# Performance work log

Measured on AMD Instinct MI355X. Metric: run time of the kernel, lower is better.

The kernel has to match this reference:

```python
import jax, jax.numpy as jnp
import numpy as np

N = 8192
D = 2048      # input_dim
DH = 1024     # input_dim // r
DO = 1024     # output_dim

def setup_inputs() -> dict:
    key = jax.random.key(0)
    ks = jax.random.split(key, 11)
    s_in = 1.0 / np.sqrt(D)
    s_h = 1.0 / np.sqrt(DH)
    return {
        "O0": jax.random.normal(ks[0], (N, D), dtype=jnp.float32),
        "Ww": jax.random.uniform(ks[1], (DH, D), jnp.float32, -s_in, s_in),
        "Wb": jax.random.uniform(ks[2], (DH,), jnp.float32, -s_in, s_in),
        "Uw": jax.random.uniform(ks[3], (DH, D), jnp.float32, -s_in, s_in),
        "Ub": jax.random.uniform(ks[4], (DH,), jnp.float32, -s_in, s_in),
        "Hw": jax.random.uniform(ks[5], (DH, D), jnp.float32, -s_in, s_in),
        "Hb": jax.random.uniform(ks[6], (DH,), jnp.float32, -s_in, s_in),
        "fc0w": jax.random.uniform(ks[7], (D, DH), jnp.float32, -s_h, s_h),
        "fc0b": jax.random.uniform(ks[8], (D,), jnp.float32, -s_h, s_h),
        "fc1w": jax.random.uniform(ks[9], (DO, D), jnp.float32, -s_in, s_in),
        "fc1b": jax.random.uniform(ks[10], (DO,), jnp.float32, -s_in, s_in),
    }

def reference(O0, Ww, Wb, Uw, Ub, Hw, Hb, fc0w, fc0b, fc1w, fc1b):
    q = O0 @ Ww.T + Wb              # [N, DH]
    k = O0 @ Uw.T + Ub              # [N, DH]
    v = O0 @ Hw.T + Hb              # [N, DH]
    scores = q @ k.T                # [N, N], unscaled as in the original
    R1 = jax.nn.softmax(scores, axis=1)
    ctx = R1 @ v                    # [N, DH]
    O1 = O0 + (ctx @ fc0w.T + fc0b) # residual, [N, D]
    O2 = O1 @ fc1w.T + fc1b         # [N, DO]
    return (O1, O2)
```

## Files before the change

kernel.cpp:

```cpp
#include <hip/hip_runtime.h>
#include <cstdint>
#include <cstddef>

typedef _Float16 f16;
typedef _Float16 f16x8 __attribute__((ext_vector_type(8)));
typedef _Float16 f16x4 __attribute__((ext_vector_type(4)));
typedef float    f32x4 __attribute__((ext_vector_type(4)));

template <int V> struct IC { static constexpr int v = V; };

template <int CTRL>
__device__ __forceinline__ float dppf(float x) {
  union { float f; int i; } u, r;
  u.f = x;
  r.i = __builtin_amdgcn_update_dpp(0, u.i, CTRL, 0xF, 0xF, true);
  return r.f;
}

__global__ __launch_bounds__(256) void cvt_f32_f16(const float* __restrict__ in,
                                                   f16* __restrict__ out, int n) {
  int i = (blockIdx.x * 256 + threadIdx.x) * 4;
  if (i < n) {
    float4 v = *(const float4*)(in + i);
    f16x4 h; h[0] = (f16)v.x; h[1] = (f16)v.y; h[2] = (f16)v.z; h[3] = (f16)v.w;
    *(f16x4*)(out + i) = h;
  }
}

__global__ __launch_bounds__(256) void cvt5_f32_f16(
    const float* __restrict__ i0, const float* __restrict__ i1,
    const float* __restrict__ i2, const float* __restrict__ i3,
    const float* __restrict__ i4, f16* __restrict__ out, int nper) {
  const int bpr = nper >> 10;
  const int r = blockIdx.x / bpr;
  const int b = blockIdx.x - r * bpr;
  const float* in = r == 0 ? i0 : r == 1 ? i1 : r == 2 ? i2 : r == 3 ? i3 : i4;
  int i = (b * 256 + threadIdx.x) * 4;
  float4 v = *(const float4*)(in + i);
  f16x4 h; h[0] = (f16)v.x; h[1] = (f16)v.y; h[2] = (f16)v.z; h[3] = (f16)v.w;
  *(f16x4*)(out + (size_t)r * nper + i) = h;
}

__global__ __launch_bounds__(256) void transpose_f16(const f16* __restrict__ in,
                                                     int ldi,
                                                     f16* __restrict__ out,
                                                     int R, int C) {
  __shared__ f16 tile[64][65];
  const int r0 = blockIdx.y * 64, c0 = blockIdx.x * 64;
  const int t = threadIdx.x;
#pragma unroll
  for (int p = 0; p < 2; p++) {
    int s = t + p * 256;
    int r = s >> 3, q = s & 7;
    const int kl = ((r & 3) << 4) + (r >> 2);
    f16x8 v = *(const f16x8*)(in + (size_t)(r0 + kl) * ldi + c0 + q * 8);
#pragma unroll
    for (int e = 0; e < 8; e++) tile[r][q * 8 + e] = v[e];
  }
  __syncthreads();
#pragma unroll
  for (int p = 0; p < 2; p++) {
    int s = t + p * 256;
    int r = s >> 3, q = s & 7;
    f16x8 v;
#pragma unroll
    for (int e = 0; e < 8; e++) v[e] = tile[q * 8 + e][r];
    *(f16x8*)(out + (size_t)(c0 + r) * R + r0 + q * 8) = v;
  }
}

template <int MODE>
__global__ __launch_bounds__(512, 2) void gemm256(
    const f16* __restrict__ A, const f16* __restrict__ B,
    int M, int N, int K, int lda, int ldb,
    const float* __restrict__ bias,
    f16* __restrict__ outH, int ldo,
    float* __restrict__ statsM, float* __restrict__ statsS, int sld,
    const float* __restrict__ alphaT,
    const float* __restrict__ resid, int ldr,
    float* __restrict__ outF, int ldof) {
  __shared__ f16 lA[2][2][128 * 64];
  __shared__ f16 lB[2][2][128 * 64];
  __shared__ float lAl[2][256];

  const int t = threadIdx.x;
  const int wave = t >> 6, lane = t & 63;
  const int wr = wave >> 2, wc = wave & 3;
  const int quad = lane >> 4, l16 = lane & 15;
  const int rc = lane >> 3;
  const int kcs = (lane & 7) ^ rc;

  const int nwg = gridDim.x * gridDim.y;
  const int bid = blockIdx.y * gridDim.x + blockIdx.x;
  const int sb = (bid & 7) * (nwg >> 3) + (bid >> 3);
  const int bx = sb % gridDim.x, by = sb / gridDim.x;
  const int m0 = by * 256, n0 = bx * 256;
  const int nk = K >> 6;

  const f16* Abase = A + (size_t)m0 * lda;
  const f16* Bbase = B + (size_t)n0 * ldb;

  auto stageA = [&](int tau, int h) {
    if (tau >= nk) return;
    const f16* src = Abase + (size_t)(h * 128 + rc) * lda + tau * 64 + kcs * 8;
    f16* dstu = &lA[tau & 1][h][0];
#pragma unroll
    for (int j = 0; j < 2; j++) {
      const int sl = j * 8 + wave;
      __builtin_amdgcn_global_load_lds(
          (const __attribute__((address_space(1))) void*)(src + (size_t)sl * 8 * lda),
          (__attribute__((address_space(3))) void*)(dstu + sl * 512), 16, 0, 0);
    }
  };
  auto stageB = [&](int tau, int h) {
    if (tau >= nk) return;
    const f16* src = Bbase + (size_t)(h * 128 + rc) * ldb + tau * 64 + kcs * 8;
    f16* dstu = &lB[tau & 1][h][0];
#pragma unroll
    for (int j = 0; j < 2; j++) {
      const int sl = j * 8 + wave;
      __builtin_amdgcn_global_load_lds(
          (const __attribute__((address_space(1))) void*)(src + (size_t)sl * 8 * ldb),
          (__attribute__((address_space(3))) void*)(dstu + sl * 512), 16, 0, 0);
    }
  };
  auto stageAl = [&](int tau) {
    if constexpr (MODE == 2) {
      if (tau >= nk) return;
      __builtin_amdgcn_global_load_lds(
          (const __attribute__((address_space(1))) void*)(alphaT + (size_t)tau * M + m0 + lane * 4),
          (__attribute__((address_space(3))) void*)(&lAl[tau & 1][0]), 16, 0, 0);
    }
  };

  f32x4 acc[2][4][2][2];
#pragma unroll
  for (int mh = 0; mh < 2; mh++)
#pragma unroll
    for (int i = 0; i < 4; i++)
#pragma unroll
      for (int nh = 0; nh < 2; nh++)
#pragma unroll
        for (int j = 0; j < 2; j++)
#pragma unroll
          for (int e = 0; e < 4; e++) acc[mh][i][nh][j][e] = 0.0f;

  f16x8 af[4][2];
  f16x8 bf[2][2][2];

  auto readA = [&](auto BUFC, auto MHC) {
    constexpr int buf = decltype(BUFC)::v;
    constexpr int mh = decltype(MHC)::v;
#pragma unroll
    for (int i = 0; i < 4; i++) {
      const int r = i * 32 + wr * 16 + l16;
#pragma unroll
      for (int s = 0; s < 2; s++) {
        const int p = ((s * 4 + quad) ^ (l16 & 7)) * 8;
        af[i][s] = *(const f16x8*)(&lA[buf][mh][r * 64 + p]);
      }
      if constexpr (MODE == 2) {
        const f16 ah = (f16)lAl[buf][mh * 128 + r];
        af[i][0] = af[i][0] * ah;
        af[i][1] = af[i][1] * ah;
      }
    }
  };
  auto readB = [&](auto BUFC, auto NHC) {
    constexpr int buf = decltype(BUFC)::v;
    constexpr int nh = decltype(NHC)::v;
    const int hb = wc >> 1;
#pragma unroll
    for (int j = 0; j < 2; j++) {
      const int r = (wc & 1) * 64 + nh * 32 + j * 16 + l16;
#pragma unroll
      for (int s = 0; s < 2; s++) {
        const int p = ((s * 4 + quad) ^ (l16 & 7)) * 8;
        bf[nh][j][s] = *(const f16x8*)(&lB[buf][hb][r * 64 + p]);
      }
    }
  };
  auto mfmaQ = [&](auto MHC, auto NHC) {
    constexpr int mh = decltype(MHC)::v;
    constexpr int nh = decltype(NHC)::v;
    __builtin_amdgcn_s_setprio(1);
#pragma unroll
    for (int i = 0; i < 4; i++)
#pragma unroll
      for (int j = 0; j < 2; j++)
#pragma unroll
        for (int s = 0; s < 2; s++)
          acc[mh][i][nh][j] = __builtin_amdgcn_mfma_f32_16x16x32_f16(
              af[i][s], bf[nh][j][s], acc[mh][i][nh][j], 0, 0, 0);
    __builtin_amdgcn_s_setprio(0);
  };

  auto tileGo = [&](auto BUFC, int tt) {
    stageA(tt + 1, 0);
    stageB(tt + 1, 0);
    stageA(tt + 1, 1);
    stageB(tt + 1, 1);
    stageAl(tt + 1);
    readA(BUFC, IC<0>{});
    readB(BUFC, IC<0>{});
    mfmaQ(IC<0>{}, IC<0>{});
    readB(BUFC, IC<1>{});
    mfmaQ(IC<0>{}, IC<1>{});
    readA(BUFC, IC<1>{});
    mfmaQ(IC<1>{}, IC<1>{});
    mfmaQ(IC<1>{}, IC<0>{});
    asm volatile("s_waitcnt vmcnt(0)" ::: "memory");
    __builtin_amdgcn_s_barrier();
  };

  stageA(0, 0); stageB(0, 0); stageA(0, 1); stageB(0, 1); stageAl(0);
  asm volatile("s_waitcnt vmcnt(0)" ::: "memory");
  __builtin_amdgcn_s_barrier();

  for (int tt = 0; tt < nk; tt += 2) {
    tileGo(IC<0>{}, tt);
    tileGo(IC<1>{}, tt + 1);
  }

  const int colb = n0 + wc * 64 + l16;
  float bv[4];
  if constexpr (MODE == 0 || MODE == 3 || MODE == 4) {
#pragma unroll
    for (int c = 0; c < 4; c++) bv[c] = bias[colb + c * 16];
  }
#pragma unroll
  for (int mh = 0; mh < 2; mh++) {
#pragma unroll
    for (int i = 0; i < 4; i++) {
#pragma unroll
      for (int e = 0; e < 4; e++) {
        const int gr = m0 + mh * 128 + i * 32 + wr * 16 + quad * 4 + e;
        const float v0 = acc[mh][i][0][0][e];
        const float v1 = acc[mh][i][0][1][e];
        const float v2 = acc[mh][i][1][0][e];
        const float v3 = acc[mh][i][1][1][e];
        if constexpr (MODE == 1) {
          float mx = fmaxf(fmaxf(v0, v1), fmaxf(v2, v3));
          mx = fmaxf(mx, dppf<0xB1>(mx));
          mx = fmaxf(mx, dppf<0x4E>(mx));
          mx = fmaxf(mx, __shfl_xor(mx, 4));
          mx = fmaxf(mx, __shfl_xor(mx, 8));
          float e0 = __expf(v0 - mx);
          float e1 = __expf(v1 - mx);
          float e2 = __expf(v2 - mx);
          float e3 = __expf(v3 - mx);
          float sm = (e0 + e1) + (e2 + e3);
          sm += dppf<0xB1>(sm);
          sm += dppf<0x4E>(sm);
          sm += __shfl_xor(sm, 4);
          sm += __shfl_xor(sm, 8);
          if (l16 == 0) {
            statsM[(size_t)gr * sld + (bx * 4 + wc)] = mx;
            statsS[(size_t)gr * sld + (bx * 4 + wc)] = sm;
          }
          f16x4 pk;
          pk[0] = (f16)e0; pk[1] = (f16)e1; pk[2] = (f16)e2; pk[3] = (f16)e3;
          *(f16x4*)(outH + (size_t)gr * ldo + n0 + wc * 64 + l16 * 4) = pk;
        } else if constexpr (MODE == 0) {
          f16* rp = outH + (size_t)gr * ldo + colb;
          rp[0]  = (f16)(v0 + bv[0]);
          rp[16] = (f16)(v1 + bv[1]);
          rp[32] = (f16)(v2 + bv[2]);
          rp[48] = (f16)(v3 + bv[3]);
        } else if constexpr (MODE == 2) {
          f16* rp = outH + (size_t)gr * ldo + colb;
          rp[0]  = (f16)v0;
          rp[16] = (f16)v1;
          rp[32] = (f16)v2;
          rp[48] = (f16)v3;
        } else if constexpr (MODE == 3) {
          float* rf = outF + (size_t)gr * ldof + colb;
          const float* rr = resid + (size_t)gr * ldr + colb;
          f16* rh = outH + (size_t)gr * ldo + colb;
          float o0 = v0 + bv[0] + rr[0];
          float o1 = v1 + bv[1] + rr[16];
          float o2 = v2 + bv[2] + rr[32];
          float o3 = v3 + bv[3] + rr[48];
          rf[0] = o0; rf[16] = o1; rf[32] = o2; rf[48] = o3;
          rh[0] = (f16)o0; rh[16] = (f16)o1; rh[32] = (f16)o2; rh[48] = (f16)o3;
        } else {
          float* rf = outF + (size_t)gr * ldof + colb;
          rf[0]  = v0 + bv[0];
          rf[16] = v1 + bv[1];
          rf[32] = v2 + bv[2];
          rf[48] = v3 + bv[3];
        }
      }
    }
  }
}

template <int MODE>
__global__ __launch_bounds__(512, 2) void gemmN128(
    const f16* __restrict__ A, const f16* __restrict__ B,
    int M, int N, int K, int lda, int ldb,
    const float* __restrict__ bias,
    f16* __restrict__ outH, int ldo,
    const float* __restrict__ alphaT,
    float* __restrict__ outF, int ldof) {
  __shared__ f16 lA[2][2][128 * 64];
  __shared__ f16 lB[2][128 * 64];
  __shared__ float lAl[2][256];

  const int t = threadIdx.x;
  const int wave = t >> 6, lane = t & 63;
  const int wr = wave >> 1, wc = wave & 1;
  const int quad = lane >> 4, l16 = lane & 15;
  const int rc = lane >> 3;
  const int kcs = (lane & 7) ^ rc;

  const int nwg = gridDim.x * gridDim.y;
  const int bid = blockIdx.y * gridDim.x + blockIdx.x;
  const int sb = (bid & 7) * (nwg >> 3) + (bid >> 3);
  const int bx = sb % gridDim.x, by = sb / gridDim.x;
  const int m0 = by * 256, n0 = bx * 128;
  const int nk = K >> 6;

  const f16* Abase = A + (size_t)m0 * lda;
  const f16* Bbase = B + (size_t)n0 * ldb;

  auto stageA = [&](int tau, int h) {
    if (tau >= nk) return;
    const f16* src = Abase + (size_t)(h * 128 + rc) * lda + tau * 64 + kcs * 8;
    f16* dstu = &lA[tau & 1][h][0];
#pragma unroll
    for (int j = 0; j < 2; j++) {
      const int sl = j * 8 + wave;
      __builtin_amdgcn_global_load_lds(
          (const __attribute__((address_space(1))) void*)(src + (size_t)sl * 8 * lda),
          (__attribute__((address_space(3))) void*)(dstu + sl * 512), 16, 0, 0);
    }
  };
  auto stageB = [&](int tau) {
    if (tau >= nk) return;
    const f16* src = Bbase + (size_t)rc * ldb + tau * 64 + kcs * 8;
    f16* dstu = &lB[tau & 1][0];
#pragma unroll
    for (int j = 0; j < 2; j++) {
      const int sl = j * 8 + wave;
      __builtin_amdgcn_global_load_lds(
          (const __attribute__((address_space(1))) void*)(src + (size_t)sl * 8 * ldb),
          (__attribute__((address_space(3))) void*)(dstu + sl * 512), 16, 0, 0);
    }
  };
  auto stageAl = [&](int tau) {
    if constexpr (MODE == 2) {
      if (tau >= nk) return;
      __builtin_amdgcn_global_load_lds(
          (const __attribute__((address_space(1))) void*)(alphaT + (size_t)tau * M + m0 + lane * 4),
          (__attribute__((address_space(3))) void*)(&lAl[tau & 1][0]), 16, 0, 0);
    }
  };

  f32x4 acc[4][2][2];
#pragma unroll
  for (int i = 0; i < 4; i++)
#pragma unroll
    for (int nh = 0; nh < 2; nh++)
#pragma unroll
      for (int j = 0; j < 2; j++)
#pragma unroll
        for (int e = 0; e < 4; e++) acc[i][nh][j][e] = 0.0f;

  f16x8 af[4][2];
  f16x8 bf[2][2][2];
  const int ha = wr >> 1;

  auto readA = [&](auto BUFC) {
    constexpr int buf = decltype(BUFC)::v;
#pragma unroll
    for (int i = 0; i < 4; i++) {
      const int r = (wr & 1) * 64 + i * 16 + l16;
#pragma unroll
      for (int s = 0; s < 2; s++) {
        const int p = ((s * 4 + quad) ^ (l16 & 7)) * 8;
        af[i][s] = *(const f16x8*)(&lA[buf][ha][r * 64 + p]);
      }
      if constexpr (MODE == 2) {
        const f16 ah = (f16)lAl[buf][wr * 64 + i * 16 + l16];
        af[i][0] = af[i][0] * ah;
        af[i][1] = af[i][1] * ah;
      }
    }
  };
  auto readB = [&](auto BUFC, auto NHC) {
    constexpr int buf = decltype(BUFC)::v;
    constexpr int nh = decltype(NHC)::v;
#pragma unroll
    for (int j = 0; j < 2; j++) {
      const int r = wc * 64 + nh * 32 + j * 16 + l16;
#pragma unroll
      for (int s = 0; s < 2; s++) {
        const int p = ((s * 4 + quad) ^ (l16 & 7)) * 8;
        bf[nh][j][s] = *(const f16x8*)(&lB[buf][r * 64 + p]);
      }
    }
  };
  auto mfmaQ = [&](auto NHC) {
    constexpr int nh = decltype(NHC)::v;
    __builtin_amdgcn_s_setprio(1);
#pragma unroll
    for (int i = 0; i < 4; i++)
#pragma unroll
      for (int j = 0; j < 2; j++)
#pragma unroll
        for (int s = 0; s < 2; s++)
          acc[i][nh][j] = __builtin_amdgcn_mfma_f32_16x16x32_f16(
              af[i][s], bf[nh][j][s], acc[i][nh][j], 0, 0, 0);
    __builtin_amdgcn_s_setprio(0);
  };

  auto tileGo = [&](auto BUFC, int tt) {
    stageA(tt + 1, 0);
    stageA(tt + 1, 1);
    stageB(tt + 1);
    stageAl(tt + 1);
    readA(BUFC);
    readB(BUFC, IC<0>{});
    mfmaQ(IC<0>{});
    readB(BUFC, IC<1>{});
    mfmaQ(IC<1>{});
    asm volatile("s_waitcnt vmcnt(0)" ::: "memory");
    __builtin_amdgcn_s_barrier();
  };

  stageA(0, 0); stageA(0, 1); stageB(0); stageAl(0);
  asm volatile("s_waitcnt vmcnt(0)" ::: "memory");
  __builtin_amdgcn_s_barrier();

  for (int tt = 0; tt < nk; tt += 2) {
    tileGo(IC<0>{}, tt);
    tileGo(IC<1>{}, tt + 1);
  }

  float bv[2][2];
  if constexpr (MODE == 0 || MODE == 4) {
#pragma unroll
    for (int nh = 0; nh < 2; nh++)
#pragma unroll
      for (int j = 0; j < 2; j++)
        bv[nh][j] = bias[n0 + wc * 64 + nh * 32 + j * 16 + l16];
  }
#pragma unroll
  for (int i = 0; i < 4; i++) {
#pragma unroll
    for (int e = 0; e < 4; e++) {
      const int gr = m0 + wr * 64 + i * 16 + quad * 4 + e;
#pragma unroll
      for (int nh = 0; nh < 2; nh++) {
#pragma unroll
        for (int j = 0; j < 2; j++) {
          const int col = n0 + wc * 64 + nh * 32 + j * 16 + l16;
          const float v = acc[i][nh][j][e];
          if constexpr (MODE == 2) {
            outH[(size_t)gr * ldo + col] = (f16)v;
          } else if constexpr (MODE == 0) {
            outH[(size_t)gr * ldo + col] = (f16)(v + bv[nh][j]);
          } else {
            outF[(size_t)gr * ldof + col] = v + bv[nh][j];
          }
        }
      }
    }
  }
}

__global__ __launch_bounds__(256) void alpha_from_stats(
    const float* __restrict__ sM, const float* __restrict__ sS,
    float* __restrict__ aT, int rows) {
  __shared__ float alph[128][65];
  const int t = threadIdx.x;
  const int r = t >> 2, j = t & 3;
  const int row = blockIdx.x * 64 + r;
  const float* pm = sM + (size_t)row * 128 + j * 32;
  const float* ps = sS + (size_t)row * 128 + j * 32;
  float mv[32];
  float mx = -1e30f;
#pragma unroll
  for (int c = 0; c < 32; c++) { mv[c] = pm[c]; mx = fmaxf(mx, mv[c]); }
  mx = fmaxf(mx, __shfl_xor(mx, 1));
  mx = fmaxf(mx, __shfl_xor(mx, 2));
  float ev[32];
  float sum = 0.0f;
#pragma unroll
  for (int c = 0; c < 32; c++) {
    ev[c] = __expf(mv[c] - mx);
    sum += ev[c] * ps[c];
  }
  sum += __shfl_xor(sum, 1);
  sum += __shfl_xor(sum, 2);
  const float rl = 1.0f / sum;
#pragma unroll
  for (int c = 0; c < 32; c++) alph[j * 32 + c][r] = ev[c] * rl;
  __syncthreads();
  const int wid = t >> 6, rr = t & 63;
#pragma unroll
  for (int c = 0; c < 32; c++) {
    const int tg = c * 4 + wid;
    aT[(size_t)tg * rows + blockIdx.x * 64 + rr] = alph[tg][rr];
  }
}

extern "C" void kernel_launch(void* const* d_in, const int* in_sizes, int n_in,
                              void* d_out, int out_size, void* d_ws, size_t ws_size,
                              hipStream_t stream) {
  const float* O0   = (const float*)d_in[0];
  const float* Ww   = (const float*)d_in[1];
  const float* Wb   = (const float*)d_in[2];
  const float* Uw   = (const float*)d_in[3];
  const float* Ub   = (const float*)d_in[4];
  const float* Hw   = (const float*)d_in[5];
  const float* Hb   = (const float*)d_in[6];
  const float* fc0w = (const float*)d_in[7];
  const float* fc0b = (const float*)d_in[8];
  const float* fc1w = (const float*)d_in[9];
  const float* fc1b = (const float*)d_in[10];

  const int N = 8192, D = 2048, DH = 1024, DO = 1024;
  const int NQKV = 3 * DH;

  char* w = (char*)d_ws;
  f16* Wwh   = (f16*)w; w += (size_t)DH * D * 2;
  f16* Uwh   = (f16*)w; w += (size_t)DH * D * 2;
  f16* Hwh   = (f16*)w; w += (size_t)DH * D * 2;
  f16* fc0wh = (f16*)w; w += (size_t)D * DH * 2;
  f16* fc1wh = (f16*)w; w += (size_t)DO * D * 2;
  float* aT  = (float*)w; w += (size_t)128 * N * 4;
  char* un = w; w += (size_t)N * DH * 2;
  float* statsM = (float*)un;
  float* statsS = statsM + (size_t)N * 128;
  f16* ctxh = (f16*)un;
  float* biasC = (float*)w; w += (size_t)NQKV * 4;
  w = (char*)(((uintptr_t)w + 255) & ~(uintptr_t)255);
  f16* Sb = (f16*)w;

  f16* oh   = (f16*)d_out;
  f16* qkv  = oh;
  f16* qh   = qkv;
  f16* kh   = qkv + DH;
  f16* vh   = qkv + 2 * DH;
  f16* O0h  = oh + (size_t)N * NQKV;
  f16* vT   = O0h + (size_t)N * D;
  f16* O1h  = Sb;

  {
    int nper = DH * D;
    cvt5_f32_f16<<<5 * (nper / 1024), 256, 0, stream>>>(
        Ww, Uw, Hw, fc0w, fc1w, Wwh, nper);
    cvt_f32_f16<<<(N * D) / 1024, 256, 0, stream>>>(O0, O0h, N * D);
    hipMemcpyAsync(biasC,          Wb, DH * 4, hipMemcpyDeviceToDevice, stream);
    hipMemcpyAsync(biasC + DH,     Ub, DH * 4, hipMemcpyDeviceToDevice, stream);
    hipMemcpyAsync(biasC + 2 * DH, Hb, DH * 4, hipMemcpyDeviceToDevice, stream);
  }

  gemmN128<0><<<dim3(NQKV / 128, N / 256), 512, 0, stream>>>(
      O0h, Wwh, N, NQKV, D, D, D, biasC, qkv, NQKV, nullptr, nullptr, 0);

  transpose_f16<<<dim3(DH / 64, N / 64), 256, 0, stream>>>(vh, NQKV, vT, N, DH);

  gemm256<1><<<dim3(N / 256, N / 256), 512, 0, stream>>>(
      qh, kh, N, N, DH, NQKV, NQKV, nullptr, Sb, N,
      statsM, statsS, 128, nullptr, nullptr, 0, nullptr, 0);

  alpha_from_stats<<<N / 64, 256, 0, stream>>>(statsM, statsS, aT, N);

  gemmN128<2><<<dim3(DH / 128, N / 256), 512, 0, stream>>>(
      Sb, vT, N, DH, N, N, N, nullptr, ctxh, DH, aT, nullptr, 0);

  gemm256<3><<<dim3(D / 256, N / 256), 512, 0, stream>>>(
      ctxh, fc0wh, N, D, DH, DH, DH, fc0b, O1h, D,
      nullptr, nullptr, 0, nullptr, O0, D, (float*)d_out, D);

  gemmN128<4><<<dim3(DO / 128, N / 256), 512, 0, stream>>>(
      O1h, fc1wh, N, DO, D, D, D, fc1b, nullptr, 0, nullptr,
      (float*)d_out + (size_t)N * D, DO);
}
```

Before: 772.0 us.

## Split-barrier pipelining in gemm256 and triple-buffered LDS pipeline in gemmN128

In gemm256, the next tile's loads are issued B-first, and a partial vmcnt wait plus barrier moves to the middle of the tile, so the second half's LDS data arrives while the first-half MFMAs run. The alpha staging and the unused MODE 0/2 paths are dropped from gemm256. gemmN128 switches from double to triple buffering with a prefetch distance of two, using partial vmcnt waits to hide global-to-LDS latency at the cost of more LDS. Block swizzling now assigns contiguous column chunks per XCD when the grid is wide, for better L2 locality.

```diff
diff --git a/kernel.cpp b/kernel.cpp
--- a/kernel.cpp
+++ b/kernel.cpp
@@ -81,7 +81,6 @@
     float* __restrict__ outF, int ldof) {
   __shared__ f16 lA[2][2][128 * 64];
   __shared__ f16 lB[2][2][128 * 64];
-  __shared__ float lAl[2][256];
 
   const int t = threadIdx.x;
   const int wave = t >> 6, lane = t & 63;
@@ -92,8 +91,16 @@
 
   const int nwg = gridDim.x * gridDim.y;
   const int bid = blockIdx.y * gridDim.x + blockIdx.x;
-  const int sb = (bid & 7) * (nwg >> 3) + (bid >> 3);
-  const int bx = sb % gridDim.x, by = sb / gridDim.x;
+  const int xcd = bid & 7, idx = bid >> 3;
+  int bx, by;
+  if (gridDim.x >= 16 && (gridDim.x & 7) == 0) {
+    const int cpx = gridDim.x >> 3;
+    bx = xcd * cpx + idx % cpx;
+    by = idx / cpx;
+  } else {
+    const int sb = xcd * (nwg >> 3) + idx;
+    bx = sb % gridDim.x; by = sb / gridDim.x;
+  }
   const int m0 = by * 256, n0 = bx * 256;
   const int nk = K >> 6;
 
@@ -124,14 +131,6 @@
           (__attribute__((address_space(3))) void*)(dstu + sl * 512), 16, 0, 0);
     }
   };
-  auto stageAl = [&](int tau) {
-    if constexpr (MODE == 2) {
-      if (tau >= nk) return;
-      __builtin_amdgcn_global_load_lds(
-          (const __attribute__((address_space(1))) void*)(alphaT + (size_t)tau * M + m0 + lane * 4),
-          (__attribute__((address_space(3))) void*)(&lAl[tau & 1][0]), 16, 0, 0);
-    }
-  };
 
   f32x4 acc[2][4][2][2];
 #pragma unroll
@@ -158,11 +157,6 @@
       for (int s = 0; s < 2; s++) {
         const int p = ((s * 4 + quad) ^ (l16 & 7)) * 8;
         af[i][s] = *(const f16x8*)(&lA[buf][mh][r * 64 + p]);
-      }
-      if constexpr (MODE == 2) {
-        const f16 ah = (f16)lAl[buf][mh * 128 + r];
-        af[i][0] = af[i][0] * ah;
-        af[i][1] = af[i][1] * ah;
       }
     }
   };
@@ -195,31 +189,37 @@
     __builtin_amdgcn_s_setprio(0);
   };
 
-  auto tileGo = [&](auto BUFC, int tt) {
-    stageA(tt + 1, 0);
-    stageB(tt + 1, 0);
-    stageA(tt + 1, 1);
-    stageB(tt + 1, 1);
-    stageAl(tt + 1);
+  auto tileGo = [&](auto BUFC, int tt, bool last) {
+    if (!last) {
+      stageB(tt + 1, 0);
+      stageB(tt + 1, 1);
+      stageA(tt + 1, 0);
+      stageA(tt + 1, 1);
+    }
     readA(BUFC, IC<0>{});
     readB(BUFC, IC<0>{});
     mfmaQ(IC<0>{}, IC<0>{});
     readB(BUFC, IC<1>{});
     mfmaQ(IC<0>{}, IC<1>{});
+    if (last) { asm volatile("s_waitcnt vmcnt(0)" ::: "memory"); }
+    else      { asm volatile("s_waitcnt vmcnt(8)" ::: "memory"); }
+    __builtin_amdgcn_s_barrier();
     readA(BUFC, IC<1>{});
     mfmaQ(IC<1>{}, IC<1>{});
     mfmaQ(IC<1>{}, IC<0>{});
-    asm volatile("s_waitcnt vmcnt(0)" ::: "memory");
-    __builtin_amdgcn_s_barrier();
-  };
-
-  stageA(0, 0); stageB(0, 0); stageA(0, 1); stageB(0, 1); stageAl(0);
+    if (!last) {
+      asm volatile("s_waitcnt vmcnt(2)" ::: "memory");
+      __builtin_amdgcn_s_barrier();
+    }
+  };
+
+  stageB(0, 0); stageB(0, 1); stageA(0, 0); stageA(0, 1);
   asm volatile("s_waitcnt vmcnt(0)" ::: "memory");
   __builtin_amdgcn_s_barrier();
 
   for (int tt = 0; tt < nk; tt += 2) {
-    tileGo(IC<0>{}, tt);
-    tileGo(IC<1>{}, tt + 1);
+    tileGo(IC<0>{}, tt, false);
+    tileGo(IC<1>{}, tt + 1, tt + 2 >= nk);
   }
 
   const int colb = n0 + wc * 64 + l16;
@@ -261,18 +261,6 @@
           f16x4 pk;
           pk[0] = (f16)e0; pk[1] = (f16)e1; pk[2] = (f16)e2; pk[3] = (f16)e3;
           *(f16x4*)(outH + (size_t)gr * ldo + n0 + wc * 64 + l16 * 4) = pk;
-        } else if constexpr (MODE == 0) {
-          f16* rp = outH + (size_t)gr * ldo + colb;
-          rp[0]  = (f16)(v0 + bv[0]);
-          rp[16] = (f16)(v1 + bv[1]);
-          rp[32] = (f16)(v2 + bv[2]);
-          rp[48] = (f16)(v3 + bv[3]);
-        } else if constexpr (MODE == 2) {
-          f16* rp = outH + (size_t)gr * ldo + colb;
-          rp[0]  = (f16)v0;
-          rp[16] = (f16)v1;
-          rp[32] = (f16)v2;
-          rp[48] = (f16)v3;
         } else if constexpr (MODE == 3) {
           float* rf = outF + (size_t)gr * ldof + colb;
           const float* rr = resid + (size_t)gr * ldr + colb;
@@ -303,9 +291,9 @@
     f16* __restrict__ outH, int ldo,
     const float* __restrict__ alphaT,
     float* __restrict__ outF, int ldof) {
-  __shared__ f16 lA[2][2][128 * 64];
-  __shared__ f16 lB[2][128 * 64];
-  __shared__ float lAl[2][256];
+  __shared__ f16 lA[3][2][128 * 64];
+  __shared__ f16 lB[3][128 * 64];
+  __shared__ float lAl[3][256];
 
   const int t = threadIdx.x;
   const int wave = t >> 6, lane = t & 63;
@@ -318,42 +306,42 @@
   const int bid = blockIdx.y * gridDim.x + blockIdx.x;
   const int sb = (bid & 7) * (nwg >> 3) + (bid >> 3);
   const int bx = sb % gridDim.x, by = sb / gridDim.x;
-  const int m0 = by * 256, n0 = bx * 128;
+  (void)bx;
+  const int m0 = by * 256, n0 = (sb % gridDim.x) * 128;
   const int nk = K >> 6;
 
   const f16* Abase = A + (size_t)m0 * lda;
   const f16* Bbase = B + (size_t)n0 * ldb;
 
-  auto stageA = [&](int tau, int h) {
+  auto stageT = [&](int tau, int b) {
     if (tau >= nk) return;
-    const f16* src = Abase + (size_t)(h * 128 + rc) * lda + tau * 64 + kcs * 8;
-    f16* dstu = &lA[tau & 1][h][0];
-#pragma unroll
-    for (int j = 0; j < 2; j++) {
-      const int sl = j * 8 + wave;
-      __builtin_amdgcn_global_load_lds(
-          (const __attribute__((address_space(1))) void*)(src + (size_t)sl * 8 * lda),
-          (__attribute__((address_space(3))) void*)(dstu + sl * 512), 16, 0, 0);
-    }
-  };
-  auto stageB = [&](int tau) {
-    if (tau >= nk) return;
-    const f16* src = Bbase + (size_t)rc * ldb + tau * 64 + kcs * 8;
-    f16* dstu = &lB[tau & 1][0];
-#pragma unroll
-    for (int j = 0; j < 2; j++) {
-      const int sl = j * 8 + wave;
-      __builtin_amdgcn_global_load_lds(
-          (const __attribute__((address_space(1))) void*)(src + (size_t)sl * 8 * ldb),
-          (__attribute__((address_space(3))) void*)(dstu + sl * 512), 16, 0, 0);
-    }
-  };
-  auto stageAl = [&](int tau) {
+#pragma unroll
+    for (int h = 0; h < 2; h++) {
+      const f16* src = Abase + (size_t)(h * 128 + rc) * lda + tau * 64 + kcs * 8;
+      f16* dstu = &lA[b][h][0];
+#pragma unroll
+      for (int j = 0; j < 2; j++) {
+        const int sl = j * 8 + wave;
+        __builtin_amdgcn_global_load_lds(
+            (const __attribute__((address_space(1))) void*)(src + (size_t)sl * 8 * lda),
+            (__attribute__((address_space(3))) void*)(dstu + sl * 512), 16, 0, 0);
+      }
+    }
+    {
+      const f16* src = Bbase + (size_t)rc * ldb + tau * 64 + kcs * 8;
+      f16* dstu = &lB[b][0];
+#pragma unroll
+      for (int j = 0; j < 2; j++) {
+        const int sl = j * 8 + wave;
+        __builtin_amdgcn_global_load_lds(
+            (const __attribute__((address_space(1))) void*)(src + (size_t)sl * 8 * ldb),
+            (__attribute__((address_space(3))) void*)(dstu + sl * 512), 16, 0, 0);
+      }
+    }
     if constexpr (MODE == 2) {
-      if (tau >= nk) return;
       __builtin_amdgcn_global_load_lds(
           (const __attribute__((address_space(1))) void*)(alphaT + (size_t)tau * M + m0 + lane * 4),
-          (__attribute__((address_space(3))) void*)(&lAl[tau & 1][0]), 16, 0, 0);
+          (__attribute__((address_space(3))) void*)(&lAl[b][0]), 16, 0, 0);
     }
   };
 
@@ -371,33 +359,33 @@
   f16x8 bf[2][2][2];
   const int ha = wr >> 1;
 
-  auto readA = [&](auto BUFC) {
-    constexpr int buf = decltype(BUFC)::v;
+  auto readA = [&](int b) {
+    const f16* la = &lA[b][0][0] + ha * (128 * 64);
 #pragma unroll
     for (int i = 0; i < 4; i++) {
       const int r = (wr & 1) * 64 + i * 16 + l16;
 #pragma unroll
       for (int s = 0; s < 2; s++) {
         const int p = ((s * 4 + quad) ^ (l16 & 7)) * 8;
-        af[i][s] = *(const f16x8*)(&lA[buf][ha][r * 64 + p]);
+        af[i][s] = *(const f16x8*)(la + r * 64 + p);
       }
       if constexpr (MODE == 2) {
-        const f16 ah = (f16)lAl[buf][wr * 64 + i * 16 + l16];
+        const f16 ah = (f16)lAl[b][wr * 64 + i * 16 + l16];
         af[i][0] = af[i][0] * ah;
         af[i][1] = af[i][1] * ah;
       }
     }
   };
-  auto readB = [&](auto BUFC, auto NHC) {
-    constexpr int buf = decltype(BUFC)::v;
+  auto readB = [&](int b, auto NHC) {
     constexpr int nh = decltype(NHC)::v;
+    const f16* lb = &lB[b][0];
 #pragma unroll
     for (int j = 0; j < 2; j++) {
       const int r = wc * 64 + nh * 32 + j * 16 + l16;
 #pragma unroll
       for (int s = 0; s < 2; s++) {
         const int p = ((s * 4 + quad) ^ (l16 & 7)) * 8;
-        bf[nh][j][s] = *(const f16x8*)(&lB[buf][r * 64 + p]);
+        bf[nh][j][s] = *(const f16x8*)(lb + r * 64 + p);
       }
     }
   };
@@ -414,29 +402,35 @@
               af[i][s], bf[nh][j][s], acc[i][nh][j], 0, 0, 0);
     __builtin_amdgcn_s_setprio(0);
   };
-
-  auto tileGo = [&](auto BUFC, int tt) {
-    stageA(tt + 1, 0);
-    stageA(tt + 1, 1);
-    stageB(tt + 1);
-    stageAl(tt + 1);
-    readA(BUFC);
-    readB(BUFC, IC<0>{});
+  auto computeT = [&](int b) {
+    readA(b);
+    readB(b, IC<0>{});
     mfmaQ(IC<0>{});
-    readB(BUFC, IC<1>{});
+    readB(b, IC<1>{});
     mfmaQ(IC<1>{});
-    asm volatile("s_waitcnt vmcnt(0)" ::: "memory");
+  };
+
+  stageT(0, 0);
+  stageT(1, 1);
+  if constexpr (MODE == 2) { asm volatile("s_waitcnt vmcnt(7)" ::: "memory"); }
+  else                     { asm volatile("s_waitcnt vmcnt(6)" ::: "memory"); }
+  __builtin_amdgcn_s_barrier();
+
+  int cc = 0;
+  for (int tt = 0; tt < nk - 2; ++tt) {
+    int b2 = cc + 2; if (b2 >= 3) b2 -= 3;
+    stageT(tt + 2, b2);
+    computeT(cc);
+    if constexpr (MODE == 2) { asm volatile("s_waitcnt vmcnt(7)" ::: "memory"); }
+    else                     { asm volatile("s_waitcnt vmcnt(6)" ::: "memory"); }
     __builtin_amdgcn_s_barrier();
-  };
-
-  stageA(0, 0); stageA(0, 1); stageB(0); stageAl(0);
+    cc = cc + 1; if (cc == 3) cc = 0;
+  }
+  computeT(cc);
   asm volatile("s_waitcnt vmcnt(0)" ::: "memory");
   __builtin_amdgcn_s_barrier();
-
-  for (int tt = 0; tt < nk; tt += 2) {
-    tileGo(IC<0>{}, tt);
-    tileGo(IC<1>{}, tt + 1);
-  }
+  cc = cc + 1; if (cc == 3) cc = 0;
+  computeT(cc);
 
   float bv[2][2];
   if constexpr (MODE == 0 || MODE == 4) {
@@ -548,6 +542,8 @@
   f16* vT   = O0h + (size_t)N * D;
   f16* O1h  = Sb;
 
+  (void)Uwh; (void)Hwh;
+
   {
     int nper = DH * D;
     cvt5_f32_f16<<<5 * (nper / 1024), 256, 0, stream>>>(
```

Result: slower. 792.6 us (+2.7%).
